# Optimization experiments

Measured on AMD Instinct MI355X. Metric: run time of the kernel, lower is better.

Reference implementation:

```python
import jax, jax.numpy as jnp
import numpy as np

N_QUBITS = 8          # == hidden_dim
DIM = 2 ** N_QUBITS   # statevector size
EMBED = 512
VOCAB = 50257
SEQ = 128
BATCH = 256


def _cnot_chain_perm(n):
    # CNOT(w,w+1) for w in 0..n-2, then CNOT(n-1,0); wire 0 = MSB.
    f = np.arange(2 ** n)
    pairs = [(w, w + 1) for w in range(n - 1)] + [(n - 1, 0)]
    for c, t in pairs:
        cbit = (f >> (n - 1 - c)) & 1
        f = f ^ (cbit << (n - 1 - t))
    inv = np.empty_like(f)
    inv[f] = np.arange(2 ** n)
    return inv

_PERM_INV = jnp.asarray(_cnot_chain_perm(N_QUBITS))
# signs[j, k] = <j|Z_k|j> = 1 - 2*bit_k(j), wire 0 = MSB
_j = np.arange(DIM)[:, None]
_SIGNS = jnp.asarray(1.0 - 2.0 * ((_j >> (N_QUBITS - 1 - np.arange(N_QUBITS))) & 1), dtype=jnp.float32)


def qlayer(y, theta):
    """RX(y_i) encoder + trainable RX(theta_i) (same axis -> RX(y+theta)),
    CNOT ring, PauliZ expectation per wire.  y: (B, n) -> (B, n)."""
    half = 0.5 * (y + theta)
    c = jnp.cos(half).astype(jnp.complex64)
    s = (-1j) * jnp.sin(half).astype(jnp.complex64)
    B = y.shape[0]
    state = jnp.ones((B, 1), jnp.complex64)
    for w in range(N_QUBITS):  # fixed small structural loop (kron build)
        amp = jnp.stack([c[:, w], s[:, w]], axis=1)  # (B, 2)
        state = (state[:, :, None] * amp[:, None, :]).reshape(B, -1)
    state = state[:, _PERM_INV]                       # apply CNOT ring
    probs = jnp.real(state * jnp.conj(state))         # (B, 2^n)
    return probs @ _SIGNS                             # (B, n)


def setup_inputs() -> dict:
    key = jax.random.key(0)
    ks = jax.random.split(key, 16)
    d_in = EMBED + N_QUBITS
    inp = {
        "sentence": jax.random.randint(ks[0], (SEQ, BATCH), 0, VOCAB),
        "features": jax.random.normal(ks[1], (BATCH, N_QUBITS), jnp.float32),
        "emb_table": 0.02 * jax.random.normal(ks[2], (VOCAB, EMBED), jnp.float32),
        "W_f": 0.05 * jax.random.normal(ks[3], (N_QUBITS, d_in), jnp.float32),
        "b_f": jnp.zeros((N_QUBITS,), jnp.float32),
        "W_i": 0.05 * jax.random.normal(ks[4], (N_QUBITS, d_in), jnp.float32),
        "b_i": jnp.zeros((N_QUBITS,), jnp.float32),
        "W_u": 0.05 * jax.random.normal(ks[5], (N_QUBITS, d_in), jnp.float32),
        "b_u": jnp.zeros((N_QUBITS,), jnp.float32),
        "W_o": 0.05 * jax.random.normal(ks[6], (N_QUBITS, d_in), jnp.float32),
        "b_o": jnp.zeros((N_QUBITS,), jnp.float32),
        "th_f": jax.random.normal(ks[7], (N_QUBITS,), jnp.float32),
        "th_i": jax.random.normal(ks[8], (N_QUBITS,), jnp.float32),
        "th_u": jax.random.normal(ks[9], (N_QUBITS,), jnp.float32),
        "th_o": jax.random.normal(ks[10], (N_QUBITS,), jnp.float32),
    }
    return inp


def reference(sentence, features, emb_table, W_f, b_f, W_i, b_i, W_u, b_u,
              W_o, b_o, th_f, th_i, th_u, th_o):
    embeds = emb_table[sentence]               # (T, B, E)
    B = embeds.shape[1]
    h0 = jnp.zeros((B, N_QUBITS), jnp.float32)
    c0 = jnp.zeros((B, N_QUBITS), jnp.float32)

    def step(carry, xt):
        hx, cx = carry
        comb = jnp.concatenate([xt, hx], axis=1)          # (B, E+H)
        f = jax.nn.sigmoid(qlayer(comb @ W_f.T + b_f, th_f))
        i = jax.nn.sigmoid(qlayer(comb @ W_i.T + b_i, th_i))
        g = jnp.tanh(qlayer(comb @ W_u.T + b_u, th_u))
        o = jax.nn.sigmoid(qlayer(comb @ W_o.T + b_o, th_o))
        cx = f * cx + i * g
        hx = o * jnp.tanh(cx)
        return (hx, cx), hx

    (hx, cx), outs = jax.lax.scan(step, (h0, c0), embeds)
    cls_input = outs[-1]                        # lstm_out[-1]: (B, H)
    return cls_input
```

## Files before the change

kernel.cpp:

```cpp
#include <hip/hip_runtime.h>
#include <hip/hip_bf16.h>

#define NQ     8
#define SEQL   128
#define BATCHN 256
#define EMBED  512
#define DIN    520
#define GSTR   32
#define GBSTR  40
#define INV2PI 0.15915494309189535f
#define WROW   524

typedef __attribute__((ext_vector_type(8))) short  bf16x8;
typedef __attribute__((ext_vector_type(4))) float  f32x4;
typedef unsigned int uint2v __attribute__((ext_vector_type(2)));

__device__ __forceinline__ bf16x8 cvt8(float4 u, float4 v) {
    union { unsigned w[4]; bf16x8 v8; } r;
    asm("v_cvt_pk_bf16_f32 %0, %1, %2" : "=v"(r.w[0]) : "v"(u.x), "v"(u.y));
    asm("v_cvt_pk_bf16_f32 %0, %1, %2" : "=v"(r.w[1]) : "v"(u.z), "v"(u.w));
    asm("v_cvt_pk_bf16_f32 %0, %1, %2" : "=v"(r.w[2]) : "v"(v.x), "v"(v.y));
    asm("v_cvt_pk_bf16_f32 %0, %1, %2" : "=v"(r.w[3]) : "v"(v.z), "v"(v.w));
    return r.v8;
}

#define DPP_QP(a,b,c,d) ((a)|((b)<<2)|((c)<<4)|((d)<<6))
#define DPP_SHL(n) (0x100+(n))
#define DPP_SHR(n) (0x110+(n))
#define DPP_ROR(n) (0x120+(n))

template<int CTRL>
__device__ __forceinline__ float updpf(float old_, float src) {
    return __int_as_float(__builtin_amdgcn_update_dpp(
        __float_as_int(old_), __float_as_int(src), CTRL, 0xF, 0xF, false));
}

__device__ __forceinline__ float xor16f(float x) {
    unsigned xu = (unsigned)__float_as_int(x);
    uint2v r = __builtin_amdgcn_permlane16_swap(xu, xu, false, false);
    return __int_as_float((int)(r.x ^ r.y ^ xu));
}

__device__ __forceinline__ float frcp(float x) { return __builtin_amdgcn_rcpf(x); }
__device__ __forceinline__ float fexp2(float x) { return __builtin_amdgcn_exp2f(x); }

#define LOG2E  1.4426950408889634f
#define LOG2E2 2.8853900817779268f

#define QSTEP(GV) do {                                                        \
    float sA = fmaf(H[0],Whp[0],fmaf(H[1],Whp[1],fmaf(H[2],Whp[2],H[3]*Whp[3]))); \
    float sB = fmaf(H[4],Whp[4],fmaf(H[5],Whp[5],fmaf(H[6],Whp[6],H[7]*Whp[7]))); \
    float cs = __builtin_amdgcn_cosf((GV) + sA + sB);                         \
    float p = cs, s;                                                          \
    s = updpf<DPP_SHR(1)>(1.0f, p); p *= (m1 ? s : 1.0f);                     \
    s = updpf<DPP_SHR(2)>(1.0f, p); p *= (m2 ? s : 1.0f);                     \
    s = updpf<DPP_SHR(4)>(1.0f, p); p *= (m4 ? s : 1.0f);                     \
    float v = jz ? 1.0f : cs;                                                 \
    v *= updpf<DPP_QP(1,0,3,2)>(v, v);                                        \
    v *= updpf<DPP_QP(2,3,0,1)>(v, v);                                        \
    float xl = updpf<DPP_SHL(4)>(v, v);                                       \
    float xr = updpf<DPP_SHR(4)>(v, v);                                       \
    v *= (m4 ? xr : xl);                                                      \
    float qv = jz ? v : p;                                                    \
    float act = fmaf(sk, frcp(1.0f + fexp2(ek * qv)), ok);                    \
    float A_  = act;                                                          \
    float B8  = updpf<DPP_ROR(8)>(A_, A_);                                    \
    float C16 = xor16f(A_);                                                   \
    float D24 = updpf<DPP_ROR(8)>(C16, C16);                                  \
    float fv = (g==0) ? A_ : (g==1) ? B8 : (g==2) ? C16 : D24;                \
    float iv = (g==1) ? A_ : (g==0) ? B8 : (g==3) ? C16 : D24;                \
    float uv = (g==2) ? A_ : (g==3) ? B8 : (g==0) ? C16 : D24;                \
    float ov = (g==3) ? A_ : (g==2) ? B8 : (g==1) ? C16 : D24;                \
    c_own = fmaf(fv, c_own, iv * uv);                                         \
    float tc = fmaf(-2.0f, frcp(1.0f + fexp2(LOG2E2 * c_own)), 1.0f);         \
    h_own = ov * tc;                                                          \
    H[0] = h_own;                                                             \
    H[1] = updpf<DPP_QP(1,0,3,2)>(H[0], H[0]);                                \
    H[2] = updpf<DPP_QP(2,3,0,1)>(H[0], H[0]);                                \
    H[3] = updpf<DPP_QP(2,3,0,1)>(H[1], H[1]);                                \
    _Pragma("unroll")                                                         \
    for (int rr = 0; rr < 4; ++rr) {                                          \
        float yl = updpf<DPP_SHL(4)>(H[rr], H[rr]);                           \
        float yr = updpf<DPP_SHR(4)>(H[rr], H[rr]);                           \
        H[4 + rr] = m4 ? yr : yl;                                             \
    }                                                                         \
} while (0)

#define PRODUCE(DST, CH) do {                                                 \
    int tok_ = sent[((CH) * 16 + lm) * BATCHN + b];                           \
    const float* ar_ = emb + (size_t)tok_ * EMBED;                            \
    float4 ua[16], va[16];                                                    \
    _Pragma("unroll")                                                         \
    for (int kc = 0; kc < 16; ++kc) {                                         \
        ua[kc] = *reinterpret_cast<const float4*>(ar_ + kc * 32 + q * 8);     \
        va[kc] = *reinterpret_cast<const float4*>(ar_ + kc * 32 + q * 8 + 4); \
    }                                                                         \
    f32x4 acc0 = {0.f,0.f,0.f,0.f};                                           \
    f32x4 acc1 = {0.f,0.f,0.f,0.f};                                           \
    _Pragma("unroll")                                                         \
    for (int kc = 0; kc < 16; ++kc) {                                         \
        bf16x8 a_ = cvt8(ua[kc], va[kc]);                                     \
        const int kl_ = kc * 32 + q * 8;                                      \
        bf16x8 b0_ = *reinterpret_cast<const bf16x8*>(&Wlds[lm][kl_]);        \
        bf16x8 b1_ = *reinterpret_cast<const bf16x8*>(&Wlds[16 + lm][kl_]);   \
        acc0 = __builtin_amdgcn_mfma_f32_16x16x32_bf16(a_, b0_, acc0, 0,0,0); \
        acc1 = __builtin_amdgcn_mfma_f32_16x16x32_bf16(a_, b1_, acc1, 0,0,0); \
    }                                                                         \
    _Pragma("unroll")                                                         \
    for (int r_ = 0; r_ < 4; ++r_) {                                          \
        (DST)[(4*q + r_) * GBSTR + lm]      = fmaf(acc0[r_], INV2PI, bc0);    \
        (DST)[(4*q + r_) * GBSTR + 16 + lm] = fmaf(acc1[r_], INV2PI, bc1);    \
    }                                                                         \
} while (0)

__global__ __launch_bounds__(128, 1)
void k_fused(const int* __restrict__ sent, const float* __restrict__ emb,
             const float* __restrict__ Wf, const float* __restrict__ Wi,
             const float* __restrict__ Wu, const float* __restrict__ Wo,
             const float* __restrict__ bf, const float* __restrict__ bi,
             const float* __restrict__ bu, const float* __restrict__ bo,
             const float* __restrict__ thf, const float* __restrict__ thi,
             const float* __restrict__ thu, const float* __restrict__ tho,
             float* __restrict__ out)
{
    __shared__ short Wlds[32][WROW];
    __shared__ float gbuf[2][16 * GBSTR];

    const int tid = threadIdx.x;
    const int b   = blockIdx.x;
    const bool producer = (tid >= 64);
    const int l32 = tid & 31;
    const int g   = l32 >> 3;
    const int j   = l32 & 7;
    const int lm  = tid & 15;
    const int q   = (tid >> 4) & 3;

    {
        const int c = tid & 31, seg = tid >> 5;
        const int gg = c >> 3, jj = c & 7;
        const float* W = (gg==0) ? Wf : (gg==1) ? Wi : (gg==2) ? Wu : Wo;
        const float* src = W + (size_t)jj * DIN + seg * 128;
        #pragma unroll
        for (int p = 0; p < 16; ++p) {
            float4 u = *reinterpret_cast<const float4*>(src + p * 8);
            float4 v = *reinterpret_cast<const float4*>(src + p * 8 + 4);
            *reinterpret_cast<bf16x8*>(&Wlds[c][seg * 128 + p * 8]) = cvt8(u, v);
        }
    }

    float Whp[8], H[8];
    float c_own = 0.f, h_own = 0.f;
    float bc0 = 0.f, bc1 = 0.f;
    bool  m1 = false, m2 = false, m4 = false, jz = false;
    float ek = 0.f, sk = 0.f, ok = 0.f;

    if (producer) {
        const int g0 = lm >> 3, j0 = lm & 7;
        const float* B0 = (g0==0) ? bf  : bi;
        const float* T0 = (g0==0) ? thf : thi;
        bc0 = (B0[j0] + T0[j0]) * INV2PI;
        const float* B1 = (g0==0) ? bu  : bo;
        const float* T1 = (g0==0) ? thu : tho;
        bc1 = (B1[j0] + T1[j0]) * INV2PI;
    } else {
        const float* Wsel = (g==0) ? Wf : (g==1) ? Wi : (g==2) ? Wu : Wo;
        #pragma unroll
        for (int rr = 0; rr < 8; ++rr) {
            Whp[rr] = Wsel[j * DIN + EMBED + (j ^ rr)] * INV2PI;
            H[rr]   = 0.f;
        }
        m1 = (j >= 1); m2 = (j >= 2); m4 = (j >= 4); jz = (j == 0);
        const bool isU = (g == 2);
        ek = isU ? LOG2E2 : -LOG2E;
        sk = isU ? -2.0f  : 1.0f;
        ok = isU ? 1.0f   : 0.0f;
    }
    __syncthreads();

    if (producer) PRODUCE(&gbuf[0][0], 0);
    __syncthreads();

    #pragma unroll 1
    for (int c = 0; c < 8; ++c) {
        if (producer) {
            if (c < 7) PRODUCE(&gbuf[(c + 1) & 1][0], c + 1);
        } else {
            const float* gc = &gbuf[c & 1][l32];
            float n0 = gc[0];
            #pragma unroll
            for (int s = 0; s < 16; ++s) {
                float nn = (s < 15) ? gc[(s + 1) * GBSTR] : 0.f;
                QSTEP(n0);
                n0 = nn;
            }
        }
        __syncthreads();
    }

    if (tid < 8) out[b * NQ + tid] = h_own;
}

extern "C" void kernel_launch(void* const* d_in, const int* in_sizes, int n_in,
                              void* d_out, int out_size, void* d_ws, size_t ws_size,
                              hipStream_t stream)
{
    const int*   sent = (const int*)  d_in[0];
    const float* emb  = (const float*)d_in[2];
    const float* Wf   = (const float*)d_in[3];
    const float* bf   = (const float*)d_in[4];
    const float* Wi   = (const float*)d_in[5];
    const float* bi   = (const float*)d_in[6];
    const float* Wu   = (const float*)d_in[7];
    const float* bu   = (const float*)d_in[8];
    const float* Wo   = (const float*)d_in[9];
    const float* bo   = (const float*)d_in[10];
    const float* thf  = (const float*)d_in[11];
    const float* thi  = (const float*)d_in[12];
    const float* thu  = (const float*)d_in[13];
    const float* tho  = (const float*)d_in[14];
    float* out = (float*)d_out;

    k_fused<<<BATCHN, 128, 0, stream>>>(sent, emb, Wf, Wi, Wu, Wo,
                                        bf, bi, bu, bo,
                                        thf, thi, thu, tho, out);
}
```

Measured before the change: 35.92 us.

## Remap gate lanes to 16-lane rows and exchange gates via permlane swaps

Consumer lanes are remapped so each gate occupies its own 16-lane row, with the 8 hidden units duplicated in the upper half of the row. The four gate activations are now exchanged with permlane16/permlane32 swaps instead of DPP row rotates. Because DPP row shifts now stay inside a gate row, the select masks in the prefix-product scan are dropped. All 16 gate pre-activations are also loaded from LDS before the step loop. The intent is to shorten the per-step serial dependency chain of the recurrence. Lanes 8-15 of each row compute unused values, and the scan is only correct for lanes 0-7.

```diff
diff --git a/kernel.cpp b/kernel.cpp
--- a/kernel.cpp
+++ b/kernel.cpp
@@ -27,7 +27,6 @@
 #define DPP_QP(a,b,c,d) ((a)|((b)<<2)|((c)<<4)|((d)<<6))
 #define DPP_SHL(n) (0x100+(n))
 #define DPP_SHR(n) (0x110+(n))
-#define DPP_ROR(n) (0x120+(n))
 
 template<int CTRL>
 __device__ __forceinline__ float updpf(float old_, float src) {
@@ -40,6 +39,11 @@
     uint2v r = __builtin_amdgcn_permlane16_swap(xu, xu, false, false);
     return __int_as_float((int)(r.x ^ r.y ^ xu));
 }
+__device__ __forceinline__ float xor32f(float x) {
+    unsigned xu = (unsigned)__float_as_int(x);
+    uint2v r = __builtin_amdgcn_permlane32_swap(xu, xu, false, false);
+    return __int_as_float((int)(r.x ^ r.y ^ xu));
+}
 
 __device__ __forceinline__ float frcp(float x) { return __builtin_amdgcn_rcpf(x); }
 __device__ __forceinline__ float fexp2(float x) { return __builtin_amdgcn_exp2f(x); }
@@ -51,10 +55,10 @@
     float sA = fmaf(H[0],Whp[0],fmaf(H[1],Whp[1],fmaf(H[2],Whp[2],H[3]*Whp[3]))); \
     float sB = fmaf(H[4],Whp[4],fmaf(H[5],Whp[5],fmaf(H[6],Whp[6],H[7]*Whp[7]))); \
     float cs = __builtin_amdgcn_cosf((GV) + sA + sB);                         \
-    float p = cs, s;                                                          \
-    s = updpf<DPP_SHR(1)>(1.0f, p); p *= (m1 ? s : 1.0f);                     \
-    s = updpf<DPP_SHR(2)>(1.0f, p); p *= (m2 ? s : 1.0f);                     \
-    s = updpf<DPP_SHR(4)>(1.0f, p); p *= (m4 ? s : 1.0f);                     \
+    float p = cs;                                                             \
+    p *= updpf<DPP_SHR(1)>(1.0f, p);                                          \
+    p *= updpf<DPP_SHR(2)>(1.0f, p);                                          \
+    p *= updpf<DPP_SHR(4)>(1.0f, p);                                          \
     float v = jz ? 1.0f : cs;                                                 \
     v *= updpf<DPP_QP(1,0,3,2)>(v, v);                                        \
     v *= updpf<DPP_QP(2,3,0,1)>(v, v);                                        \
@@ -63,14 +67,14 @@
     v *= (m4 ? xr : xl);                                                      \
     float qv = jz ? v : p;                                                    \
     float act = fmaf(sk, frcp(1.0f + fexp2(ek * qv)), ok);                    \
-    float A_  = act;                                                          \
-    float B8  = updpf<DPP_ROR(8)>(A_, A_);                                    \
-    float C16 = xor16f(A_);                                                   \
-    float D24 = updpf<DPP_ROR(8)>(C16, C16);                                  \
-    float fv = (g==0) ? A_ : (g==1) ? B8 : (g==2) ? C16 : D24;                \
-    float iv = (g==1) ? A_ : (g==0) ? B8 : (g==3) ? C16 : D24;                \
-    float uv = (g==2) ? A_ : (g==3) ? B8 : (g==0) ? C16 : D24;                \
-    float ov = (g==3) ? A_ : (g==2) ? B8 : (g==1) ? C16 : D24;                \
+    float A_ = act;                                                           \
+    float B_ = xor16f(A_);                                      \
+    float C_ = xor32f(A_);                                      \
+    float D_ = xor16f(C_);                                      \
+    float fv = (g==0) ? A_ : (g==1) ? B_ : (g==2) ? C_ : D_;                  \
+    float iv = (g==0) ? B_ : (g==1) ? A_ : (g==2) ? D_ : C_;                  \
+    float uv = (g==0) ? C_ : (g==1) ? D_ : (g==2) ? A_ : B_;                  \
+    float ov = (g==0) ? D_ : (g==1) ? C_ : (g==2) ? B_ : A_;                  \
     c_own = fmaf(fv, c_own, iv * uv);                                         \
     float tc = fmaf(-2.0f, frcp(1.0f + fexp2(LOG2E2 * c_own)), 1.0f);         \
     h_own = ov * tc;                                                          \
@@ -129,9 +133,8 @@
     const int tid = threadIdx.x;
     const int b   = blockIdx.x;
     const bool producer = (tid >= 64);
-    const int l32 = tid & 31;
-    const int g   = l32 >> 3;
-    const int j   = l32 & 7;
+    const int g   = (tid >> 4) & 3;
+    const int j   = tid & 7;
     const int lm  = tid & 15;
     const int q   = (tid >> 4) & 3;
 
@@ -151,7 +154,7 @@
     float Whp[8], H[8];
     float c_own = 0.f, h_own = 0.f;
     float bc0 = 0.f, bc1 = 0.f;
-    bool  m1 = false, m2 = false, m4 = false, jz = false;
+    bool  m4 = false, jz = false;
     float ek = 0.f, sk = 0.f, ok = 0.f;
 
     if (producer) {
@@ -169,7 +172,7 @@
             Whp[rr] = Wsel[j * DIN + EMBED + (j ^ rr)] * INV2PI;
             H[rr]   = 0.f;
         }
-        m1 = (j >= 1); m2 = (j >= 2); m4 = (j >= 4); jz = (j == 0);
+        m4 = (j >= 4); jz = (j == 0);
         const bool isU = (g == 2);
         ek = isU ? LOG2E2 : -LOG2E;
         sk = isU ? -2.0f  : 1.0f;
@@ -180,19 +183,19 @@
     if (producer) PRODUCE(&gbuf[0][0], 0);
     __syncthreads();
 
+    const int gidx = g * 8 + j;
+
     #pragma unroll 1
     for (int c = 0; c < 8; ++c) {
         if (producer) {
             if (c < 7) PRODUCE(&gbuf[(c + 1) & 1][0], c + 1);
         } else {
-            const float* gc = &gbuf[c & 1][l32];
-            float n0 = gc[0];
+            const float* gc = &gbuf[c & 1][gidx];
+            float gvv[16];
             #pragma unroll
-            for (int s = 0; s < 16; ++s) {
-                float nn = (s < 15) ? gc[(s + 1) * GBSTR] : 0.f;
-                QSTEP(n0);
-                n0 = nn;
-            }
+            for (int s = 0; s < 16; ++s) gvv[s] = gc[s * GBSTR];
+            #pragma unroll
+            for (int s = 0; s < 16; ++s) QSTEP(gvv[s]);
         }
         __syncthreads();
     }
```

After: 38.30 us. +6.6%, slower.
